# Performance work log

Measured on AMD Instinct MI355X. Metric: run time of the kernel, lower is better.

The kernel has to match this reference:

```python
import jax, jax.numpy as jnp
import numpy as np

ALPHA = 0.1
DEPTH = 10

N_NODES = 100000
N_EDGES = 3200000
FEATS = 512
HIDDEN = 64
CLASSES = 32


def setup_inputs() -> dict:
    key = jax.random.key(0)
    k1, k2, k3, k4 = jax.random.split(key, 4)
    x = jax.random.normal(k1, (N_NODES, FEATS), dtype=jnp.float32)
    edges = jax.random.randint(k2, (2, N_EDGES), 0, N_NODES, dtype=jnp.int64)
    # Linear weights (stored as [in, out] so forward is x @ W + b)
    W1 = jax.random.normal(k3, (FEATS, HIDDEN), dtype=jnp.float32) * (1.0 / np.sqrt(FEATS))
    b1 = jnp.zeros((HIDDEN,), dtype=jnp.float32)
    W2 = jax.random.normal(k4, (HIDDEN, CLASSES), dtype=jnp.float32) * (1.0 / np.sqrt(HIDDEN))
    b2 = jnp.zeros((CLASSES,), dtype=jnp.float32)
    return {"x": x, "edges": edges, "W1": W1, "b1": b1, "W2": W2, "b2": b2}


def reference(x, edges, W1, b1, W2, b2):
    # Eval mode: all dropouts (feature + edge) are identity.
    n = x.shape[0]
    src, dst = edges[0], edges[1]

    # Symmetric normalization 1/sqrt(deg_src * deg_dst), degrees from in-edges.
    deg = jax.ops.segment_sum(jnp.ones_like(dst, dtype=x.dtype), dst, num_segments=n)
    deg = jnp.maximum(deg, 1.0)
    norm = jax.lax.rsqrt(deg[src] * deg[dst])  # [E]

    # MLP: feats -> hidden -> classes
    h = jax.nn.relu(x @ W1 + b1) @ W2 + b2  # [N, classes]
    h0 = h

    # APPNP propagation: x <- (1-alpha) * A_hat x + alpha * h0
    for _ in range(DEPTH):
        msg = h[src] * norm[:, None]                          # gather  [E, classes]
        agg = jax.ops.segment_sum(msg, dst, num_segments=n)   # scatter [N, classes]
        h = agg * (1.0 - ALPHA) + ALPHA * h0
    return h
```

## Files before the change

kernel.cpp:

```cpp
#include <hip/hip_runtime.h>

#define ALPHA_F 0.1f
#define DEPTH 10
#define FEATS 512
#define HID 64
#define CLS 32

__device__ __forceinline__ unsigned bf16rne(float f) {
  unsigned u = __float_as_uint(f);
  return (u + 0x7fffu + ((u >> 16) & 1u)) >> 16;
}
__device__ __forceinline__ float blo(unsigned q) { return __uint_as_float(q << 16); }
__device__ __forceinline__ float bhi(unsigned q) { return __uint_as_float(q & 0xffff0000u); }

__global__ __launch_bounds__(256) void k_deg(const int* __restrict__ dst, int E, int N,
                                             unsigned* __restrict__ deg,
                                             unsigned* __restrict__ rank) {
  int i = blockIdx.x * 256 + threadIdx.x;
  if (i >= E) return;
  int d = dst[i];
  unsigned r = 0;
  if ((unsigned)d < (unsigned)N) r = atomicAdd(&deg[d], 1u);
  rank[i] = r;
}

__global__ __launch_bounds__(1024) void k_scan(const unsigned* __restrict__ deg, int N,
                                               unsigned* __restrict__ rowst) {
  __shared__ unsigned sums[1024];
  int t = threadIdx.x;
  int chunk = (N + 1023) >> 10;
  int beg = t * chunk;
  int end = min(beg + chunk, N);
  unsigned s = 0;
  for (int i = beg; i < end; ++i) s += deg[i];
  sums[t] = s;
  __syncthreads();
  for (int off = 1; off < 1024; off <<= 1) {
    unsigned v = (t >= off) ? sums[t - off] : 0u;
    __syncthreads();
    sums[t] += v;
    __syncthreads();
  }
  unsigned pre = (t == 0) ? 0u : sums[t - 1];
  for (int i = beg; i < end; ++i) { rowst[i] = pre; pre += deg[i]; }
  if (t == 1023) rowst[N] = pre;
}

__global__ __launch_bounds__(256) void k_fill(const int* __restrict__ src,
                                              const int* __restrict__ dst,
                                              const unsigned* __restrict__ rank,
                                              const unsigned* __restrict__ rowst,
                                              int E, int N,
                                              int* __restrict__ col) {
  int e = blockIdx.x * 256 + threadIdx.x;
  if (e >= E) return;
  int s = src[e];
  int d = dst[e];
  if ((unsigned)s >= (unsigned)N || (unsigned)d >= (unsigned)N) return;
  col[rowst[d] + rank[e]] = s;
}

__global__ __launch_bounds__(256) void k_mlp(const float* __restrict__ x,
                                             const float* __restrict__ W1,
                                             const float* __restrict__ b1,
                                             const float* __restrict__ W2,
                                             const float* __restrict__ b2,
                                             const unsigned* __restrict__ deg,
                                             float* __restrict__ h0,
                                             unsigned short* __restrict__ u0,
                                             float* __restrict__ rs, int N) {
  __shared__ float XHs[128 * 68];
  __shared__ float W2s[64 * 32];
  __shared__ float b1s[64];
  __shared__ float b2s[32];
  int t = threadIdx.x;
  int m0 = blockIdx.x * 128;

  for (int i = t; i < 64 * 32; i += 256) W2s[i] = W2[i];
  if (t < 64) b1s[t] = b1[t];
  if (t < 32) b2s[t] = b2[t];

  int c4 = t & 15;
  int hg = t >> 4;
  float acc[8][4];
#pragma unroll
  for (int i = 0; i < 8; ++i)
#pragma unroll
    for (int m = 0; m < 4; ++m) acc[i][m] = 0.f;

  for (int k0 = 0; k0 < FEATS; k0 += 64) {
    __syncthreads();
#pragma unroll
    for (int j = 0; j < 8; ++j) {
      int F = j * 256 + t;
      int r = F >> 4, q = F & 15;
      int row = m0 + r;
      float4 v = make_float4(0.f, 0.f, 0.f, 0.f);
      if (row < N) v = *(const float4*)(x + (size_t)row * FEATS + k0 + q * 4);
      *(float4*)(XHs + r * 68 + q * 4) = v;
    }
    __syncthreads();
    const float* W1p = W1 + (size_t)k0 * 64;
#pragma unroll
    for (int k4 = 0; k4 < 16; ++k4) {
      int k = k4 * 4;
      float4 xv[8];
#pragma unroll
      for (int i = 0; i < 8; ++i) xv[i] = *(const float4*)(XHs + (i * 16 + hg) * 68 + k);
      float4 w[4];
#pragma unroll
      for (int j = 0; j < 4; ++j) w[j] = *(const float4*)(W1p + (size_t)(k + j) * 64 + c4 * 4);
#pragma unroll
      for (int j = 0; j < 4; ++j) {
#pragma unroll
        for (int i = 0; i < 8; ++i) {
          float xx = ((const float*)&xv[i])[j];
          acc[i][0] += xx * w[j].x;
          acc[i][1] += xx * w[j].y;
          acc[i][2] += xx * w[j].z;
          acc[i][3] += xx * w[j].w;
        }
      }
    }
  }
  __syncthreads();
#pragma unroll
  for (int i = 0; i < 8; ++i) {
    int r = i * 16 + hg;
    float4 o;
    o.x = fmaxf(acc[i][0] + b1s[c4 * 4 + 0], 0.f);
    o.y = fmaxf(acc[i][1] + b1s[c4 * 4 + 1], 0.f);
    o.z = fmaxf(acc[i][2] + b1s[c4 * 4 + 2], 0.f);
    o.w = fmaxf(acc[i][3] + b1s[c4 * 4 + 3], 0.f);
    *(float4*)(XHs + r * 68 + c4 * 4) = o;
  }
  __syncthreads();
  int cc = t & 31, g = t >> 5;
#pragma unroll
  for (int i = 0; i < 16; ++i) {
    int r = i * 8 + g;
    float s = b2s[cc];
#pragma unroll
    for (int k = 0; k < 64; ++k) s += XHs[r * 68 + k] * W2s[k * 32 + cc];
    int row = m0 + r;
    if (row < N) {
      float dv = (float)deg[row];
      float rsv = rsqrtf(fmaxf(dv, 1.0f));
      h0[(size_t)row * CLS + cc] = s;
      u0[(size_t)row * CLS + cc] = (unsigned short)bf16rne(rsv * s);
      if (cc == 0) rs[row] = rsv;
    }
  }
}

template <bool LAST>
__global__ __launch_bounds__(256) void k_prop(const unsigned* __restrict__ u_in,
                                              const float* __restrict__ h0,
                                              const float* __restrict__ rs,
                                              const unsigned* __restrict__ rowst,
                                              const int* __restrict__ col,
                                              void* __restrict__ out, int N) {
  int t = blockIdx.x * 256 + threadIdx.x;
  int node = t >> 2;
  if (node >= N) return;
  int l = t & 3;
  unsigned beg = rowst[node];
  unsigned end = rowst[node + 1];
  const uint4* up = (const uint4*)u_in + l;
  float a[8], b[8];
#pragma unroll
  for (int j = 0; j < 8; ++j) { a[j] = 0.f; b[j] = 0.f; }
  unsigned e = beg;
  for (; e + 8 <= end; e += 8) {
    int s0 = col[e + 0], s1 = col[e + 1], s2 = col[e + 2], s3 = col[e + 3];
    int s4 = col[e + 4], s5 = col[e + 5], s6 = col[e + 6], s7 = col[e + 7];
    uint4 q0 = up[(size_t)s0 * 4];
    uint4 q1 = up[(size_t)s1 * 4];
    uint4 q2 = up[(size_t)s2 * 4];
    uint4 q3 = up[(size_t)s3 * 4];
    uint4 q4 = up[(size_t)s4 * 4];
    uint4 q5 = up[(size_t)s5 * 4];
    uint4 q6 = up[(size_t)s6 * 4];
    uint4 q7 = up[(size_t)s7 * 4];
    a[0] += blo(q0.x); a[1] += bhi(q0.x); a[2] += blo(q0.y); a[3] += bhi(q0.y);
    a[4] += blo(q0.z); a[5] += bhi(q0.z); a[6] += blo(q0.w); a[7] += bhi(q0.w);
    b[0] += blo(q1.x); b[1] += bhi(q1.x); b[2] += blo(q1.y); b[3] += bhi(q1.y);
    b[4] += blo(q1.z); b[5] += bhi(q1.z); b[6] += blo(q1.w); b[7] += bhi(q1.w);
    a[0] += blo(q2.x); a[1] += bhi(q2.x); a[2] += blo(q2.y); a[3] += bhi(q2.y);
    a[4] += blo(q2.z); a[5] += bhi(q2.z); a[6] += blo(q2.w); a[7] += bhi(q2.w);
    b[0] += blo(q3.x); b[1] += bhi(q3.x); b[2] += blo(q3.y); b[3] += bhi(q3.y);
    b[4] += blo(q3.z); b[5] += bhi(q3.z); b[6] += blo(q3.w); b[7] += bhi(q3.w);
    a[0] += blo(q4.x); a[1] += bhi(q4.x); a[2] += blo(q4.y); a[3] += bhi(q4.y);
    a[4] += blo(q4.z); a[5] += bhi(q4.z); a[6] += blo(q4.w); a[7] += bhi(q4.w);
    b[0] += blo(q5.x); b[1] += bhi(q5.x); b[2] += blo(q5.y); b[3] += bhi(q5.y);
    b[4] += blo(q5.z); b[5] += bhi(q5.z); b[6] += blo(q5.w); b[7] += bhi(q5.w);
    a[0] += blo(q6.x); a[1] += bhi(q6.x); a[2] += blo(q6.y); a[3] += bhi(q6.y);
    a[4] += blo(q6.z); a[5] += bhi(q6.z); a[6] += blo(q6.w); a[7] += bhi(q6.w);
    b[0] += blo(q7.x); b[1] += bhi(q7.x); b[2] += blo(q7.y); b[3] += bhi(q7.y);
    b[4] += blo(q7.z); b[5] += bhi(q7.z); b[6] += blo(q7.w); b[7] += bhi(q7.w);
  }
  for (; e < end; ++e) {
    int s = col[e];
    uint4 q = up[(size_t)s * 4];
    a[0] += blo(q.x); a[1] += bhi(q.x); a[2] += blo(q.y); a[3] += bhi(q.y);
    a[4] += blo(q.z); a[5] += bhi(q.z); a[6] += blo(q.w); a[7] += bhi(q.w);
  }
#pragma unroll
  for (int j = 0; j < 8; ++j) a[j] += b[j];
  float rsv = rs[node];
  const float* h0p = h0 + (size_t)node * CLS + l * 8;
  float4 h0a = *(const float4*)(h0p);
  float4 h0b = *(const float4*)(h0p + 4);
  if (LAST) {
    float ca = ALPHA_F, cb = (1.0f - ALPHA_F) * rsv;
    float* op = (float*)out + (size_t)node * CLS + l * 8;
    *(float4*)(op) = make_float4(ca * h0a.x + cb * a[0], ca * h0a.y + cb * a[1],
                                 ca * h0a.z + cb * a[2], ca * h0a.w + cb * a[3]);
    *(float4*)(op + 4) = make_float4(ca * h0b.x + cb * a[4], ca * h0b.y + cb * a[5],
                                     ca * h0b.z + cb * a[6], ca * h0b.w + cb * a[7]);
  } else {
    float ca = ALPHA_F * rsv, cb = (1.0f - ALPHA_F) * rsv * rsv;
    float o0 = ca * h0a.x + cb * a[0], o1 = ca * h0a.y + cb * a[1];
    float o2 = ca * h0a.z + cb * a[2], o3 = ca * h0a.w + cb * a[3];
    float o4 = ca * h0b.x + cb * a[4], o5 = ca * h0b.y + cb * a[5];
    float o6 = ca * h0b.z + cb * a[6], o7 = ca * h0b.w + cb * a[7];
    uint4 p;
    p.x = bf16rne(o0) | (bf16rne(o1) << 16);
    p.y = bf16rne(o2) | (bf16rne(o3) << 16);
    p.z = bf16rne(o4) | (bf16rne(o5) << 16);
    p.w = bf16rne(o6) | (bf16rne(o7) << 16);
    *((uint4*)out + (size_t)node * 4 + l) = p;
  }
}

extern "C" void kernel_launch(void* const* d_in, const int* in_sizes, int n_in,
                              void* d_out, int out_size, void* d_ws, size_t ws_size,
                              hipStream_t stream) {
  const float* x = (const float*)d_in[0];
  const int* edges = (const int*)d_in[1];
  const float* W1 = (const float*)d_in[2];
  const float* b1 = (const float*)d_in[3];
  const float* W2 = (const float*)d_in[4];
  const float* b2 = (const float*)d_in[5];
  int N = in_sizes[0] / FEATS;
  int E = in_sizes[1] / 2;
  const int* src = edges;
  const int* dst = edges + E;

  char* ws = (char*)d_ws;
  auto align64 = [](size_t v) { return (v + 63) & ~(size_t)63; };
  size_t o = 0;
  unsigned* deg = (unsigned*)(ws + o);   o = align64(o + (size_t)N * 4);
  unsigned* rowst = (unsigned*)(ws + o); o = align64(o + (size_t)(N + 1) * 4);
  float* rs = (float*)(ws + o);          o = align64(o + (size_t)N * 4);
  int* col = (int*)(ws + o);             o = align64(o + (size_t)E * 4);
  float* h0 = (float*)(ws + o);          o = align64(o + (size_t)N * CLS * 4);
  unsigned* uA = (unsigned*)(ws + o);    o = align64(o + (size_t)N * CLS * 2);
  unsigned* uB = (unsigned*)(ws + o);    o = align64(o + (size_t)N * CLS * 2);
  unsigned* rank = (unsigned*)h0;

  hipMemsetAsync(deg, 0, (size_t)N * 4, stream);
  k_deg<<<(E + 255) / 256, 256, 0, stream>>>(dst, E, N, deg, rank);
  k_scan<<<1, 1024, 0, stream>>>(deg, N, rowst);
  k_fill<<<(E + 255) / 256, 256, 0, stream>>>(src, dst, rank, rowst, E, N, col);
  k_mlp<<<(N + 127) / 128, 256, 0, stream>>>(x, W1, b1, W2, b2, deg, h0,
                                             (unsigned short*)uA, rs, N);

  float* outF = (float*)d_out;
  const unsigned* uin = uA;
  for (int it = 0; it < DEPTH - 1; ++it) {
    unsigned* uo = (it & 1) ? uA : uB;
    k_prop<false><<<((N * 4) + 255) / 256, 256, 0, stream>>>(uin, h0, rs, rowst, col, uo, N);
    uin = uo;
  }
  k_prop<true><<<((N * 4) + 255) / 256, 256, 0, stream>>>(uin, h0, rs, rowst, col, outF, N);
}
```

Before: 1.244 ms.

## Reorder nodes by degree bins to balance propagation work per wavefront

Result: slower. 1.682 ms (+35.2%).

```diff
diff --git a/kernel.cpp b/kernel.cpp
--- a/kernel.cpp
+++ b/kernel.cpp
@@ -3,7 +3,6 @@
 #define ALPHA_F 0.1f
 #define DEPTH 10
 #define FEATS 512
-#define HID 64
 #define CLS 32
 
 __device__ __forceinline__ unsigned bf16rne(float f) {
@@ -24,15 +23,15 @@
   rank[i] = r;
 }
 
-__global__ __launch_bounds__(1024) void k_scan(const unsigned* __restrict__ deg, int N,
-                                               unsigned* __restrict__ rowst) {
+__global__ __launch_bounds__(1024) void k_scan(const unsigned* __restrict__ in, int N,
+                                               unsigned* __restrict__ out) {
   __shared__ unsigned sums[1024];
   int t = threadIdx.x;
   int chunk = (N + 1023) >> 10;
   int beg = t * chunk;
   int end = min(beg + chunk, N);
   unsigned s = 0;
-  for (int i = beg; i < end; ++i) s += deg[i];
+  for (int i = beg; i < end; ++i) s += in[i];
   sums[t] = s;
   __syncthreads();
   for (int off = 1; off < 1024; off <<= 1) {
@@ -42,22 +41,47 @@
     __syncthreads();
   }
   unsigned pre = (t == 0) ? 0u : sums[t - 1];
-  for (int i = beg; i < end; ++i) { rowst[i] = pre; pre += deg[i]; }
-  if (t == 1023) rowst[N] = pre;
+  for (int i = beg; i < end; ++i) { out[i] = pre; pre += in[i]; }
+  if (t == 1023) out[N] = pre;
+}
+
+__global__ __launch_bounds__(256) void k_hist(const unsigned* __restrict__ deg, int N,
+                                              unsigned* __restrict__ hist) {
+  int i = blockIdx.x * 256 + threadIdx.x;
+  if (i >= N) return;
+  atomicAdd(&hist[min(deg[i], 256u)], 1u);
+}
+
+__global__ __launch_bounds__(256) void k_perm(const unsigned* __restrict__ deg,
+                                              const unsigned* __restrict__ rowst,
+                                              unsigned* __restrict__ binoff2, int N,
+                                              unsigned* __restrict__ perm,
+                                              unsigned* __restrict__ inv,
+                                              uint2* __restrict__ be) {
+  int i = blockIdx.x * 256 + threadIdx.x;
+  if (i >= N) return;
+  unsigned d = deg[i];
+  unsigned b = min(d, 256u);
+  unsigned pos = atomicAdd(&binoff2[b], 1u);
+  perm[pos] = (unsigned)i;
+  inv[i] = pos;
+  unsigned r0 = rowst[i];
+  be[pos] = make_uint2(r0, r0 + d);
 }
 
 __global__ __launch_bounds__(256) void k_fill(const int* __restrict__ src,
                                               const int* __restrict__ dst,
                                               const unsigned* __restrict__ rank,
                                               const unsigned* __restrict__ rowst,
+                                              const unsigned* __restrict__ inv,
                                               int E, int N,
-                                              int* __restrict__ col) {
+                                              unsigned* __restrict__ col2) {
   int e = blockIdx.x * 256 + threadIdx.x;
   if (e >= E) return;
   int s = src[e];
   int d = dst[e];
   if ((unsigned)s >= (unsigned)N || (unsigned)d >= (unsigned)N) return;
-  col[rowst[d] + rank[e]] = s;
+  col2[rowst[d] + rank[e]] = inv[s];
 }
 
 __global__ __launch_bounds__(256) void k_mlp(const float* __restrict__ x,
@@ -66,38 +90,40 @@
                                              const float* __restrict__ W2,
                                              const float* __restrict__ b2,
                                              const unsigned* __restrict__ deg,
-                                             float* __restrict__ h0,
+                                             const unsigned* __restrict__ inv,
+                                             float* __restrict__ h0s,
                                              unsigned short* __restrict__ u0,
-                                             float* __restrict__ rs, int N) {
-  __shared__ float XHs[128 * 68];
+                                             float* __restrict__ rss, int N) {
+  __shared__ float XHs[64 * 65];
   __shared__ float W2s[64 * 32];
   __shared__ float b1s[64];
   __shared__ float b2s[32];
   int t = threadIdx.x;
-  int m0 = blockIdx.x * 128;
+  int m0 = blockIdx.x * 64;
 
   for (int i = t; i < 64 * 32; i += 256) W2s[i] = W2[i];
   if (t < 64) b1s[t] = b1[t];
   if (t < 32) b2s[t] = b2[t];
 
-  int c4 = t & 15;
-  int hg = t >> 4;
-  float acc[8][4];
-#pragma unroll
-  for (int i = 0; i < 8; ++i)
-#pragma unroll
-    for (int m = 0; m < 4; ++m) acc[i][m] = 0.f;
+  int c = t & 31;
+  int h = t >> 5;
+  float acc[8][2];
+#pragma unroll
+  for (int i = 0; i < 8; ++i) { acc[i][0] = 0.f; acc[i][1] = 0.f; }
 
   for (int k0 = 0; k0 < FEATS; k0 += 64) {
     __syncthreads();
 #pragma unroll
-    for (int j = 0; j < 8; ++j) {
+    for (int j = 0; j < 2; ++j) {
       int F = j * 256 + t;
-      int r = F >> 4, q = F & 15;
+      int r = F >> 3, q = F & 7;
       int row = m0 + r;
       float4 v = make_float4(0.f, 0.f, 0.f, 0.f);
-      if (row < N) v = *(const float4*)(x + (size_t)row * FEATS + k0 + q * 4);
-      *(float4*)(XHs + r * 68 + q * 4) = v;
+      if (row < N) v = *(const float4*)(x + (size_t)row * FEATS + k0 + q * 8);
+      *(float4*)(XHs + r * 64 + q * 8) = v;
+      float4 v2 = make_float4(0.f, 0.f, 0.f, 0.f);
+      if (row < N) v2 = *(const float4*)(x + (size_t)row * FEATS + k0 + q * 8 + 4);
+      *(float4*)(XHs + r * 64 + q * 8 + 4) = v2;
     }
     __syncthreads();
     const float* W1p = W1 + (size_t)k0 * 64;
@@ -106,19 +132,16 @@
       int k = k4 * 4;
       float4 xv[8];
 #pragma unroll
-      for (int i = 0; i < 8; ++i) xv[i] = *(const float4*)(XHs + (i * 16 + hg) * 68 + k);
-      float4 w[4];
-#pragma unroll
-      for (int j = 0; j < 4; ++j) w[j] = *(const float4*)(W1p + (size_t)(k + j) * 64 + c4 * 4);
+      for (int i = 0; i < 8; ++i) xv[i] = *(const float4*)(XHs + (h * 8 + i) * 64 + k);
 #pragma unroll
       for (int j = 0; j < 4; ++j) {
+        float w0 = W1p[(k + j) * 64 + c];
+        float w1 = W1p[(k + j) * 64 + c + 32];
 #pragma unroll
         for (int i = 0; i < 8; ++i) {
           float xx = ((const float*)&xv[i])[j];
-          acc[i][0] += xx * w[j].x;
-          acc[i][1] += xx * w[j].y;
-          acc[i][2] += xx * w[j].z;
-          acc[i][3] += xx * w[j].w;
+          acc[i][0] += xx * w0;
+          acc[i][1] += xx * w1;
         }
       }
     }
@@ -126,54 +149,54 @@
   __syncthreads();
 #pragma unroll
   for (int i = 0; i < 8; ++i) {
-    int r = i * 16 + hg;
-    float4 o;
-    o.x = fmaxf(acc[i][0] + b1s[c4 * 4 + 0], 0.f);
-    o.y = fmaxf(acc[i][1] + b1s[c4 * 4 + 1], 0.f);
-    o.z = fmaxf(acc[i][2] + b1s[c4 * 4 + 2], 0.f);
-    o.w = fmaxf(acc[i][3] + b1s[c4 * 4 + 3], 0.f);
-    *(float4*)(XHs + r * 68 + c4 * 4) = o;
+    int r = h * 8 + i;
+    float v0 = acc[i][0] + b1s[c];
+    float v1 = acc[i][1] + b1s[c + 32];
+    XHs[r * 65 + c] = v0 > 0.f ? v0 : 0.f;
+    XHs[r * 65 + c + 32] = v1 > 0.f ? v1 : 0.f;
   }
   __syncthreads();
-  int cc = t & 31, g = t >> 5;
-#pragma unroll
-  for (int i = 0; i < 16; ++i) {
-    int r = i * 8 + g;
+  int cc = t & 31;
+#pragma unroll
+  for (int i = 0; i < 8; ++i) {
+    int r = h * 8 + i;
     float s = b2s[cc];
 #pragma unroll
-    for (int k = 0; k < 64; ++k) s += XHs[r * 68 + k] * W2s[k * 32 + cc];
+    for (int k = 0; k < 64; ++k) s += XHs[r * 65 + k] * W2s[k * 32 + cc];
     int row = m0 + r;
     if (row < N) {
+      unsigned g = inv[row];
       float dv = (float)deg[row];
       float rsv = rsqrtf(fmaxf(dv, 1.0f));
-      h0[(size_t)row * CLS + cc] = s;
-      u0[(size_t)row * CLS + cc] = (unsigned short)bf16rne(rsv * s);
-      if (cc == 0) rs[row] = rsv;
+      h0s[(size_t)g * CLS + cc] = s;
+      u0[(size_t)g * CLS + cc] = (unsigned short)bf16rne(rsv * s);
+      if (cc == 0) rss[g] = rsv;
     }
   }
 }
 
 template <bool LAST>
 __global__ __launch_bounds__(256) void k_prop(const unsigned* __restrict__ u_in,
-                                              const float* __restrict__ h0,
-                                              const float* __restrict__ rs,
-                                              const unsigned* __restrict__ rowst,
-                                              const int* __restrict__ col,
+                                              const float* __restrict__ h0s,
+                                              const float* __restrict__ rss,
+                                              const uint2* __restrict__ be,
+                                              const unsigned* __restrict__ col2,
+                                              const unsigned* __restrict__ perm,
                                               void* __restrict__ out, int N) {
   int t = blockIdx.x * 256 + threadIdx.x;
-  int node = t >> 2;
-  if (node >= N) return;
+  int g = t >> 2;
+  if (g >= N) return;
   int l = t & 3;
-  unsigned beg = rowst[node];
-  unsigned end = rowst[node + 1];
+  uint2 brange = be[g];
+  unsigned beg = brange.x, end = brange.y;
   const uint4* up = (const uint4*)u_in + l;
   float a[8], b[8];
 #pragma unroll
   for (int j = 0; j < 8; ++j) { a[j] = 0.f; b[j] = 0.f; }
   unsigned e = beg;
   for (; e + 8 <= end; e += 8) {
-    int s0 = col[e + 0], s1 = col[e + 1], s2 = col[e + 2], s3 = col[e + 3];
-    int s4 = col[e + 4], s5 = col[e + 5], s6 = col[e + 6], s7 = col[e + 7];
+    unsigned s0 = col2[e + 0], s1 = col2[e + 1], s2 = col2[e + 2], s3 = col2[e + 3];
+    unsigned s4 = col2[e + 4], s5 = col2[e + 5], s6 = col2[e + 6], s7 = col2[e + 7];
     uint4 q0 = up[(size_t)s0 * 4];
     uint4 q1 = up[(size_t)s1 * 4];
     uint4 q2 = up[(size_t)s2 * 4];
@@ -200,19 +223,20 @@
     b[4] += blo(q7.z); b[5] += bhi(q7.z); b[6] += blo(q7.w); b[7] += bhi(q7.w);
   }
   for (; e < end; ++e) {
-    int s = col[e];
+    unsigned s = col2[e];
     uint4 q = up[(size_t)s * 4];
     a[0] += blo(q.x); a[1] += bhi(q.x); a[2] += blo(q.y); a[3] += bhi(q.y);
     a[4] += blo(q.z); a[5] += bhi(q.z); a[6] += blo(q.w); a[7] += bhi(q.w);
   }
 #pragma unroll
   for (int j = 0; j < 8; ++j) a[j] += b[j];
-  float rsv = rs[node];
-  const float* h0p = h0 + (size_t)node * CLS + l * 8;
+  float rsv = rss[g];
+  const float* h0p = h0s + (size_t)g * CLS + l * 8;
   float4 h0a = *(const float4*)(h0p);
   float4 h0b = *(const float4*)(h0p + 4);
   if (LAST) {
     float ca = ALPHA_F, cb = (1.0f - ALPHA_F) * rsv;
+    unsigned node = perm[g];
     float* op = (float*)out + (size_t)node * CLS + l * 8;
     *(float4*)(op) = make_float4(ca * h0a.x + cb * a[0], ca * h0a.y + cb * a[1],
                                  ca * h0a.z + cb * a[2], ca * h0a.w + cb * a[3]);
@@ -229,7 +253,7 @@
     p.y = bf16rne(o2) | (bf16rne(o3) << 16);
     p.z = bf16rne(o4) | (bf16rne(o5) << 16);
     p.w = bf16rne(o6) | (bf16rne(o7) << 16);
-    *((uint4*)out + (size_t)node * 4 + l) = p;
+    *((uint4*)out + (size_t)g * 4 + l) = p;
   }
 }
 
@@ -250,28 +274,41 @@
   char* ws = (char*)d_ws;
   auto align64 = [](size_t v) { return (v + 63) & ~(size_t)63; };
   size_t o = 0;
-  unsigned* deg = (unsigned*)(ws + o);   o = align64(o + (size_t)N * 4);
-  unsigned* rowst = (unsigned*)(ws + o); o = align64(o + (size_t)(N + 1) * 4);
-  float* rs = (float*)(ws + o);          o = align64(o + (size_t)N * 4);
-  int* col = (int*)(ws + o);             o = align64(o + (size_t)E * 4);
-  float* h0 = (float*)(ws + o);          o = align64(o + (size_t)N * CLS * 4);
-  unsigned* uA = (unsigned*)(ws + o);    o = align64(o + (size_t)N * CLS * 2);
-  unsigned* uB = (unsigned*)(ws + o);    o = align64(o + (size_t)N * CLS * 2);
-  unsigned* rank = (unsigned*)h0;
+  unsigned* deg = (unsigned*)(ws + o);     o = align64(o + (size_t)N * 4);
+  unsigned* rowst = (unsigned*)(ws + o);   o = align64(o + (size_t)(N + 1) * 4);
+  unsigned* hist = (unsigned*)(ws + o);    o = align64(o + 258 * 4);
+  unsigned* binoff = (unsigned*)(ws + o);  o = align64(o + 258 * 4);
+  unsigned* binoff2 = (unsigned*)(ws + o); o = align64(o + 258 * 4);
+  unsigned* perm = (unsigned*)(ws + o);    o = align64(o + (size_t)N * 4);
+  unsigned* inv = (unsigned*)(ws + o);     o = align64(o + (size_t)N * 4);
+  float* rss = (float*)(ws + o);           o = align64(o + (size_t)N * 4);
+  uint2* be = (uint2*)(ws + o);            o = align64(o + (size_t)N * 8);
+  unsigned* rank = (unsigned*)(ws + o);    o = align64(o + (size_t)E * 4);
+  unsigned* col2 = (unsigned*)(ws + o);    o = align64(o + (size_t)E * 4);
+  float* h0s = (float*)(ws + o);           o = align64(o + (size_t)N * CLS * 4);
+  unsigned* uA = (unsigned*)(ws + o);      o = align64(o + (size_t)N * CLS * 2);
+  unsigned* uB = (unsigned*)(ws + o);      o = align64(o + (size_t)N * CLS * 2);
 
   hipMemsetAsync(deg, 0, (size_t)N * 4, stream);
+  hipMemsetAsync(hist, 0, 258 * 4, stream);
   k_deg<<<(E + 255) / 256, 256, 0, stream>>>(dst, E, N, deg, rank);
   k_scan<<<1, 1024, 0, stream>>>(deg, N, rowst);
-  k_fill<<<(E + 255) / 256, 256, 0, stream>>>(src, dst, rank, rowst, E, N, col);
-  k_mlp<<<(N + 127) / 128, 256, 0, stream>>>(x, W1, b1, W2, b2, deg, h0,
-                                             (unsigned short*)uA, rs, N);
+  k_hist<<<(N + 255) / 256, 256, 0, stream>>>(deg, N, hist);
+  k_scan<<<1, 1024, 0, stream>>>(hist, 257, binoff);
+  hipMemcpyAsync(binoff2, binoff, 258 * 4, hipMemcpyDeviceToDevice, stream);
+  k_perm<<<(N + 255) / 256, 256, 0, stream>>>(deg, rowst, binoff2, N, perm, inv, be);
+  k_fill<<<(E + 255) / 256, 256, 0, stream>>>(src, dst, rank, rowst, inv, E, N, col2);
+  k_mlp<<<(N + 63) / 64, 256, 0, stream>>>(x, W1, b1, W2, b2, deg, inv, h0s,
+                                           (unsigned short*)uA, rss, N);
 
   float* outF = (float*)d_out;
   const unsigned* uin = uA;
   for (int it = 0; it < DEPTH - 1; ++it) {
     unsigned* uo = (it & 1) ? uA : uB;
-    k_prop<false><<<((N * 4) + 255) / 256, 256, 0, stream>>>(uin, h0, rs, rowst, col, uo, N);
+    k_prop<false><<<((N * 4) + 255) / 256, 256, 0, stream>>>(uin, h0s, rss, be, col2,
+                                                             perm, uo, N);
     uin = uo;
   }
-  k_prop<true><<<((N * 4) + 255) / 256, 256, 0, stream>>>(uin, h0, rs, rowst, col, outF, N);
-}
+  k_prop<true><<<((N * 4) + 255) / 256, 256, 0, stream>>>(uin, h0s, rss, be, col2,
+                                                          perm, outF, N);
+}
```
